# Kernel tuning notes

Hardware: AMD Instinct MI355X
Metric: run time of the kernel (lower is better)

## Reference

```python
import jax, jax.numpy as jnp
import numpy as np

NT = 128          # num_timesteps (reference query points)
E = 128           # embed_time
H = 128           # nhidden
NH = 1            # num_heads
F = 32            # feature_size
NS = 2            # num_states
EPS = 1e-5


def layer_norm(x, g, b):
    m = jnp.mean(x, axis=-1, keepdims=True)
    v = jnp.mean((x - m) ** 2, axis=-1, keepdims=True)
    return (x - m) * jax.lax.rsqrt(v + EPS) * g + b


def setup_inputs() -> dict:
    key = jax.random.key(0)
    ks = jax.random.split(key, 24)
    nrm = lambda k, s: (jax.random.normal(k, s) * 0.05).astype(jnp.float32)
    inp = {
        "input": jax.random.normal(ks[0], (8, F, 512), dtype=jnp.float32),
        "mask": jax.random.randint(ks[1], (8, F, 512), 0, 2).astype(jnp.float32),
        "timesteps": jnp.sort(jax.random.uniform(ks[2], (8, 512), dtype=jnp.float32), axis=-1),
        # time embedding
        "periodic_w": nrm(ks[3], (E - 1, 1)), "periodic_b": nrm(ks[4], (E - 1,)),
        "lin_w": nrm(ks[5], (1, 1)), "lin_b": nrm(ks[6], (1,)),
        # query / key projections + layer norms
        "q_w": nrm(ks[7], (E, E)), "q_b": nrm(ks[8], (E,)),
        "q_g": jnp.ones((E,), jnp.float32), "q_be": jnp.zeros((E,), jnp.float32),
        "k_w": nrm(ks[9], (E, E)), "k_b": nrm(ks[10], (E,)),
        "k_g": jnp.ones((E,), jnp.float32), "k_be": jnp.zeros((E,), jnp.float32),
        # attention_norm over h*2F channels, then output linear + LN to nhidden
        "attn_g": jnp.ones((NH * 2 * F,), jnp.float32), "attn_b": jnp.zeros((NH * 2 * F,), jnp.float32),
        "out_w": nrm(ks[11], (H, NH * 2 * F)), "out_b": nrm(ks[12], (H,)),
        "out_g": jnp.ones((H,), jnp.float32), "out_be": jnp.zeros((H,), jnp.float32),
        # GRU (torch gate order r, z, n)
        "gru_wih": nrm(ks[13], (3 * H, H)), "gru_whh": nrm(ks[14], (3 * H, H)),
        "gru_bih": nrm(ks[15], (3 * H,)), "gru_bhh": nrm(ks[16], (3 * H,)),
        # classifier MLP
        "c1_w": nrm(ks[17], (H, H)), "c1_b": nrm(ks[18], (H,)),
        "c2_w": nrm(ks[19], (H, H)), "c2_b": nrm(ks[20], (H,)),
        "c3_w": nrm(ks[21], (NS, H)), "c3_b": nrm(ks[22], (NS,)),
    }
    return inp


def time_embedding(tt, lin_w, lin_b, periodic_w, periodic_b):
    t = tt[..., None]                                   # (..., 1)
    out1 = t @ lin_w.T + lin_b                          # (..., 1)
    out2 = jnp.sin(t @ periodic_w.T + periodic_b)       # (..., E-1)
    return jnp.concatenate([out1, out2], axis=-1)       # (..., E)


def reference(input, mask, timesteps, periodic_w, periodic_b, lin_w, lin_b,
              q_w, q_b, q_g, q_be, k_w, k_b, k_g, k_be,
              attn_g, attn_b, out_w, out_b, out_g, out_be,
              gru_wih, gru_whh, gru_bih, gru_bhh,
              c1_w, c1_b, c2_w, c2_b, c3_w, c3_b):
    B = input.shape[0]
    x_in = jnp.transpose(input, (0, 2, 1))              # (B, T, F)
    m = 1.0 - jnp.transpose(mask, (0, 2, 1))            # (B, T, F)
    x_in = x_in * (m > 0).astype(x_in.dtype)
    x = jnp.concatenate([x_in, m], axis=-1)             # (B, T, 2F)
    mk = jnp.concatenate([m, m], axis=-1)               # (B, T, 2F)

    key_e = time_embedding(timesteps, lin_w, lin_b, periodic_w, periodic_b)        # (B, T, E)
    qtimes = jnp.linspace(0.0, 1.0, NT)
    query_e = time_embedding(qtimes[None], lin_w, lin_b, periodic_w, periodic_b)   # (1, NT, E)

    q = layer_norm(query_e @ q_w.T + q_b, q_g, q_be)    # (1, NT, E)
    k = layer_norm(key_e @ k_w.T + k_b, k_g, k_be)      # (B, T, E)

    etk = E // NH
    q = q.reshape(1, NT, NH, etk).transpose(0, 2, 1, 3)         # (1, h, NT, etk)
    k = k.reshape(B, -1, NH, etk).transpose(0, 2, 1, 3)         # (B, h, T, etk)

    scores = jnp.einsum("ahqd,bhkd->bhqk", q, k) / np.sqrt(etk)  # (B, h, NT, T)
    # per-channel masked softmax over keys: (B, h, NT, T, 2F)
    logits = jnp.where(mk[:, None, None, :, :] == 0, -1e9, scores[..., None])
    p_attn = jax.nn.softmax(logits, axis=-2)
    att = jnp.sum(p_attn * x[:, None, None, :, :], axis=-2)     # (B, h, NT, 2F)

    x2 = att.transpose(0, 2, 1, 3).reshape(B, NT, NH * 2 * F)
    x2 = layer_norm(x2, attn_g, attn_b)
    out = layer_norm(x2 @ out_w.T + out_b, out_g, out_be)       # (B, NT, H)

    # GRU over the NT reference timesteps, last hidden state
    seq = out.transpose(1, 0, 2)                                # (NT, B, H)
    h0 = jnp.zeros((B, H), out.dtype)

    def gru_step(h, x_t):
        gi = x_t @ gru_wih.T + gru_bih
        gh = h @ gru_whh.T + gru_bhh
        ir, iz, inn = jnp.split(gi, 3, axis=-1)
        hr, hz, hn = jnp.split(gh, 3, axis=-1)
        r = jax.nn.sigmoid(ir + hr)
        z = jax.nn.sigmoid(iz + hz)
        n = jnp.tanh(inn + r * hn)
        h_new = (1.0 - z) * n + z * h
        return h_new, None

    h_last, _ = jax.lax.scan(gru_step, h0, seq)

    h1 = jax.nn.relu(h_last @ c1_w.T + c1_b)
    h2 = jax.nn.relu(h1 @ c2_w.T + c2_b)
    return h2 @ c3_w.T + c3_b                                   # (B, num_states) logits
```

## Files before the change

kernel.cpp:

```cpp
#include <hip/hip_runtime.h>
#include <math.h>

#define LN_EPS 1e-5f

typedef _Float16 h2v __attribute__((ext_vector_type(2)));

__device__ __forceinline__ float dot4(float4 a, float4 b) {
    return a.x*b.x + a.y*b.y + a.z*b.z + a.w*b.w;
}
__device__ __forceinline__ void fma4(float4& a, float s, float4 v) {
    a.x += s*v.x; a.y += s*v.y; a.z += s*v.z; a.w += s*v.w;
}
__device__ __forceinline__ float fast_rcp(float x) {
    return __builtin_amdgcn_rcpf(x);
}
__device__ __forceinline__ float fast_sigmoid(float x) {
    return fast_rcp(1.f + __expf(-x));
}
__device__ __forceinline__ float fast_tanh(float x) {
    return 1.f - 2.f*fast_rcp(__expf(2.f*x) + 1.f);
}
__device__ __forceinline__ float fdot2u(unsigned int a, unsigned int b, float c) {
#if __has_builtin(__builtin_amdgcn_fdot2)
    return __builtin_amdgcn_fdot2(__builtin_bit_cast(h2v, a),
                                  __builtin_bit_cast(h2v, b), c, false);
#else
    const h2v av = __builtin_bit_cast(h2v, a);
    const h2v bv = __builtin_bit_cast(h2v, b);
    return c + (float)av[0]*(float)bv[0] + (float)av[1]*(float)bv[1];
#endif
}
__device__ __forceinline__ float wsum64(float v) {
    #pragma unroll
    for (int off = 32; off > 0; off >>= 1) v += __shfl_xor(v, off);
    return v;
}
__device__ __forceinline__ float qadd_xor1(float v) {
    const int x = __builtin_amdgcn_mov_dpp(__builtin_bit_cast(int, v),
                                           0xB1 , 0xF, 0xF, true);
    return v + __builtin_bit_cast(float, x);
}

__global__ void k_embed_proj(
    const float* __restrict__ input, const float* __restrict__ mask,
    const float* __restrict__ timesteps,
    const float* __restrict__ pw, const float* __restrict__ pb,
    const float* __restrict__ lw, const float* __restrict__ lb,
    const float* __restrict__ q_w, const float* __restrict__ q_b,
    const float* __restrict__ q_g, const float* __restrict__ q_be,
    const float* __restrict__ k_w, const float* __restrict__ k_b,
    const float* __restrict__ k_g, const float* __restrict__ k_be,
    float* __restrict__ qs, float* __restrict__ kT, float2* __restrict__ xm)
{
    const int blk = blockIdx.x;
    const int tid = threadIdx.x;

    __shared__ __align__(16) float e[4][128];
    __shared__ __align__(16) float4 red[128];
    __shared__ __align__(16) float proj[4][128];
    __shared__ __align__(16) float2 tile[32][65];

    if (blk < 64) {
        const int b  = blk >> 3;
        const int t0 = (blk & 7) * 64;
        const int cg = tid >> 6;
        const int tt = tid & 63;
        #pragma unroll
        for (int c16 = 0; c16 < 16; ++c16) {
            const int c = c16*2 + cg;
            const float m = mask [(size_t)(b*32 + c)*512 + t0 + tt];
            const float x = input[(size_t)(b*32 + c)*512 + t0 + tt];
            const float mm = 1.0f - m;
            tile[c][tt] = make_float2(x*mm, mm);
        }
        __syncthreads();
        const int c2 = tid & 31;
        const int tg = tid >> 5;
        #pragma unroll
        for (int k = 0; k < 16; ++k) {
            const int t = tg*16 + k;
            xm[((size_t)b*512 + t0 + t)*32 + c2] = tile[c2][t];
        }
        return;
    }

    const bool isq = blk < 96;
    float tv[4];
    int kidx0 = 0;
    if (isq) {
        const int q0 = (blk - 64) * 4;
        #pragma unroll
        for (int r = 0; r < 4; ++r) tv[r] = (float)(q0 + r) * (1.0f/127.0f);
    } else {
        kidx0 = (blk - 96) * 4;
        #pragma unroll
        for (int r = 0; r < 4; ++r) tv[r] = timesteps[kidx0 + r];
    }

    float pwj = 0.f, pbj = 0.f;
    if (tid > 0) { pwj = pw[tid-1]; pbj = pb[tid-1]; }
    const float lw0 = lw[0], lb0 = lb[0];
    #pragma unroll
    for (int r = 0; r < 4; ++r)
        e[r][tid] = (tid == 0) ? (tv[r]*lw0 + lb0) : sinf(tv[r]*pwj + pbj);
    __syncthreads();

    const float* W  = isq ? q_w  : k_w;
    const float* Bv = isq ? q_b  : k_b;
    const float* G  = isq ? q_g  : k_g;
    const float* Be = isq ? q_be : k_be;

    {
        const int jj = tid >> 2, dc = tid & 3;
        const float4* e0 = (const float4*)(&e[0][0]);
        const float4* e1 = (const float4*)(&e[1][0]);
        const float4* e2 = (const float4*)(&e[2][0]);
        const float4* e3 = (const float4*)(&e[3][0]);
        #pragma unroll
        for (int jb = 0; jb < 4; ++jb) {
            const int j = jb*32 + jj;
            const float4* wrow = (const float4*)(W + (size_t)j*128);
            float a0=0.f, a1=0.f, a2=0.f, a3=0.f;
            #pragma unroll
            for (int k = 0; k < 8; ++k) {
                const int idx = dc + 4*k;
                const float4 w4 = wrow[idx];
                a0 += dot4(w4, e0[idx]);
                a1 += dot4(w4, e1[idx]);
                a2 += dot4(w4, e2[idx]);
                a3 += dot4(w4, e3[idx]);
            }
            a0 += __shfl_xor(a0, 1, 4); a0 += __shfl_xor(a0, 2, 4);
            a1 += __shfl_xor(a1, 1, 4); a1 += __shfl_xor(a1, 2, 4);
            a2 += __shfl_xor(a2, 1, 4); a2 += __shfl_xor(a2, 2, 4);
            a3 += __shfl_xor(a3, 1, 4); a3 += __shfl_xor(a3, 2, 4);
            if (dc == 0) {
                const float bj = Bv[j];
                proj[0][j] = a0 + bj; proj[1][j] = a1 + bj;
                proj[2][j] = a2 + bj; proj[3][j] = a3 + bj;
            }
        }
    }
    __syncthreads();

    float acc[4];
    #pragma unroll
    for (int r = 0; r < 4; ++r) acc[r] = proj[r][tid];

    red[tid] = make_float4(acc[0], acc[1], acc[2], acc[3]);
    __syncthreads();
    for (int s = 64; s > 0; s >>= 1) {
        if (tid < s) {
            float4 m = red[tid]; const float4 o = red[tid+s];
            m.x += o.x; m.y += o.y; m.z += o.z; m.w += o.w;
            red[tid] = m;
        }
        __syncthreads();
    }
    float4 mean = red[0];
    mean.x *= (1.0f/128.0f); mean.y *= (1.0f/128.0f);
    mean.z *= (1.0f/128.0f); mean.w *= (1.0f/128.0f);
    __syncthreads();
    const float d0 = acc[0]-mean.x, d1 = acc[1]-mean.y,
                d2 = acc[2]-mean.z, d3 = acc[3]-mean.w;
    red[tid] = make_float4(d0*d0, d1*d1, d2*d2, d3*d3);
    __syncthreads();
    for (int s = 64; s > 0; s >>= 1) {
        if (tid < s) {
            float4 m = red[tid]; const float4 o = red[tid+s];
            m.x += o.x; m.y += o.y; m.z += o.z; m.w += o.w;
            red[tid] = m;
        }
        __syncthreads();
    }
    float4 var = red[0];
    var.x *= (1.0f/128.0f); var.y *= (1.0f/128.0f);
    var.z *= (1.0f/128.0f); var.w *= (1.0f/128.0f);

    const float gg = G[tid], bb = Be[tid];
    const float o0 = d0*rsqrtf(var.x+LN_EPS)*gg + bb;
    const float o1 = d1*rsqrtf(var.y+LN_EPS)*gg + bb;
    const float o2 = d2*rsqrtf(var.z+LN_EPS)*gg + bb;
    const float o3 = d3*rsqrtf(var.w+LN_EPS)*gg + bb;

    if (isq) {
        const float sc = 0.08838834764831845f;
        const int q0 = (blk - 64)*4;
        qs[(size_t)(q0+0)*128 + tid] = o0*sc;
        qs[(size_t)(q0+1)*128 + tid] = o1*sc;
        qs[(size_t)(q0+2)*128 + tid] = o2*sc;
        qs[(size_t)(q0+3)*128 + tid] = o3*sc;
    } else {
        const int b = kidx0 >> 9;
        const int t = kidx0 & 511;
        *(float4*)(kT + ((size_t)(b*128 + tid))*512 + t) =
            make_float4(o0, o1, o2, o3);
    }
}

__global__ void __launch_bounds__(256) k_attn(
    const float2* __restrict__ xm,
    const float* __restrict__ qs, const float* __restrict__ kT,
    const float* __restrict__ attn_g, const float* __restrict__ attn_b,
    const float* __restrict__ out_w, const float* __restrict__ out_b,
    const float* __restrict__ out_g, const float* __restrict__ out_be,
    float* __restrict__ outm)
{
    const int b     = blockIdx.x >> 5;
    const int qbase = (blockIdx.x & 31) * 4;
    const int tid   = threadIdx.x;

    __shared__ __align__(16) float et[4][512];
    __shared__ __align__(16) float qsh[4][128];
    __shared__ __align__(16) float wsh[128*66];
    __shared__ __align__(16) float sA[4][8][32];
    __shared__ __align__(16) float aA[4][8][32];
    __shared__ __align__(16) float x2s[4][64];
    __shared__ float redC[4];

    for (int idx = tid; idx < 512; idx += 256)
        qsh[idx >> 7][idx & 127] = qs[(size_t)(qbase + (idx >> 7))*128 + (idx & 127)];
    for (int idx = tid; idx < 8192; idx += 256)
        wsh[(idx >> 6)*66 + (idx & 63)] = out_w[idx];
    __syncthreads();

    {
        const int grp = tid >> 7;
        const int tl  = tid & 127;
        const int q0  = grp*2;
        const float4* kp  = (const float4*)kT + (size_t)b*128*128 + tl;
        const float4* qa4 = (const float4*)qsh[q0];
        const float4* qb4 = (const float4*)qsh[q0+1];
        float4 a0 = make_float4(0,0,0,0), a1 = make_float4(0,0,0,0);
        float4 c0 = kp[0], c1 = kp[128], c2 = kp[256], c3 = kp[384];
        for (int c = 0; c < 32; ++c) {
            float4 n0, n1, n2, n3;
            if (c < 31) {
                const float4* kn = kp + (size_t)(4*c+4)*128;
                n0 = kn[0]; n1 = kn[128]; n2 = kn[256]; n3 = kn[384];
            }
            const float4 qa = qa4[c], qb = qb4[c];
            fma4(a0, qa.x, c0); fma4(a1, qb.x, c0);
            fma4(a0, qa.y, c1); fma4(a1, qb.y, c1);
            fma4(a0, qa.z, c2); fma4(a1, qb.z, c2);
            fma4(a0, qa.w, c3); fma4(a1, qb.w, c3);
            c0 = n0; c1 = n1; c2 = n2; c3 = n3;
        }
        a0.x = __expf(a0.x); a0.y = __expf(a0.y); a0.z = __expf(a0.z); a0.w = __expf(a0.w);
        a1.x = __expf(a1.x); a1.y = __expf(a1.y); a1.z = __expf(a1.z); a1.w = __expf(a1.w);
        ((float4*)et[q0])[tl]   = a0;
        ((float4*)et[q0+1])[tl] = a1;
    }
    __syncthreads();

    {
        const int c   = tid & 31;
        const int seg = tid >> 5;
        const float2* xp = xm + ((size_t)b*512 + seg*64)*32 + c;
        float s0=0,s1=0,s2=0,s3=0, a0=0,a1=0,a2=0,a3=0;
        #pragma unroll 4
        for (int i = 0; i < 64; ++i) {
            const float2 v = xp[(size_t)i*32];
            const int t = seg*64 + i;
            const float w0 = et[0][t]*v.y, w1 = et[1][t]*v.y;
            const float w2 = et[2][t]*v.y, w3 = et[3][t]*v.y;
            s0 += w0; s1 += w1; s2 += w2; s3 += w3;
            a0 += w0*v.x; a1 += w1*v.x; a2 += w2*v.x; a3 += w3*v.x;
        }
        sA[0][seg][c]=s0; sA[1][seg][c]=s1; sA[2][seg][c]=s2; sA[3][seg][c]=s3;
        aA[0][seg][c]=a0; aA[1][seg][c]=a1; aA[2][seg][c]=a2; aA[3][seg][c]=a3;
    }
    __syncthreads();

    {
        const int ql = tid >> 6;
        const int c2 = tid & 63;
        const int cc = c2 & 31;
        float ss = 0.f;
        #pragma unroll
        for (int g = 0; g < 8; ++g) ss += sA[ql][g][cc];
        float attv;
        if (c2 < 32) {
            float aa = 0.f;
            #pragma unroll
            for (int g = 0; g < 8; ++g) aa += aA[ql][g][cc];
            attv = (ss > 0.f) ? aa/ss : 0.f;
        } else {
            attv = (ss > 0.f) ? 1.0f : 0.0f;
        }
        const float mean = wsum64(attv) * (1.0f/64.0f);
        const float dv = attv - mean;
        const float var = wsum64(dv*dv) * (1.0f/64.0f);
        x2s[ql][c2] = dv*rsqrtf(var+LN_EPS)*attn_g[c2] + attn_b[c2];
    }
    __syncthreads();

    {
        const int jhalf = tid >> 7;
        const int j     = tid & 127;
        const int wave  = tid >> 6;
        for (int lq2 = 0; lq2 < 2; ++lq2) {
            const int ql = jhalf*2 + lq2;
            float acc = out_b[j];
            const float4* wrow = (const float4*)(wsh + j*66);
            const float4* xr   = (const float4*)x2s[ql];
            #pragma unroll
            for (int k = 0; k < 16; ++k) acc += dot4(wrow[k], xr[k]);

            float v = wsum64(acc);
            if ((tid & 63) == 0) redC[wave] = v;
            __syncthreads();
            const float mean = (redC[jhalf*2] + redC[jhalf*2+1]) * (1.0f/128.0f);
            __syncthreads();
            const float d = acc - mean;
            v = wsum64(d*d);
            if ((tid & 63) == 0) redC[wave] = v;
            __syncthreads();
            const float var = (redC[jhalf*2] + redC[jhalf*2+1]) * (1.0f/128.0f);
            outm[((size_t)b*128 + qbase + ql)*128 + j] =
                d*rsqrtf(var+LN_EPS)*out_g[j] + out_be[j];
            __syncthreads();
        }
    }
}

__global__ void k_gi(const float* __restrict__ outm,
                     const float* __restrict__ wih, const float* __restrict__ bih,
                     float* __restrict__ gi)
{
    const int qi  = blockIdx.x;
    const int tid = threadIdx.x;
    __shared__ __align__(16) float rows[8][128];
    for (int idx = tid; idx < 1024; idx += 384) {
        const int b = idx >> 7, d = idx & 127;
        rows[b][d] = outm[(size_t)(b*128+qi)*128 + d];
    }
    __syncthreads();

    const int g0 = tid >> 2, dc = tid & 3;
    #pragma unroll
    for (int gb = 0; gb < 4; ++gb) {
        const int g = gb*96 + g0;
        const float4* wrow = (const float4*)(wih + (size_t)g*128);
        float acc[8] = {0,0,0,0,0,0,0,0};
        #pragma unroll
        for (int k = 0; k < 8; ++k) {
            const int idx = dc + 4*k;
            const float4 w4 = wrow[idx];
            #pragma unroll
            for (int b = 0; b < 8; ++b)
                acc[b] += dot4(w4, ((const float4*)rows[b])[idx]);
        }
        #pragma unroll
        for (int b = 0; b < 8; ++b) {
            acc[b] += __shfl_xor(acc[b], 1, 4);
            acc[b] += __shfl_xor(acc[b], 2, 4);
        }
        if (dc == 0) {
            const float bi = bih[g];
            #pragma unroll
            for (int b = 0; b < 8; ++b)
                gi[((size_t)qi*8 + b)*384 + g] = acc[b] + bi;
        }
    }
}

__global__ void __launch_bounds__(256) k_gru_cls(
    const float* __restrict__ gi,
    const float* __restrict__ whh, const float* __restrict__ bhh,
    const float* __restrict__ c1w, const float* __restrict__ c1b,
    const float* __restrict__ c2w, const float* __restrict__ c2b,
    const float* __restrict__ c3w, const float* __restrict__ c3b,
    float* __restrict__ out)
{
    const int b   = blockIdx.x;
    const int tid = threadIdx.x;
    const int u   = tid >> 1;
    const int s   = tid & 1;

    __shared__ __align__(16) _Float16 hbuf[2][128];
    __shared__ __align__(16) float hcls[128];
    __shared__ __align__(16) float scr[256];

    unsigned int wreg[3][32];
    #pragma unroll
    for (int g = 0; g < 3; ++g) {
        const float4* wrow = (const float4*)(whh + (size_t)(g*128 + u)*128 + 64*s);
        #pragma unroll
        for (int i = 0; i < 16; ++i) {
            const float4 v = wrow[i];
            h2v p0; p0[0] = (_Float16)v.x; p0[1] = (_Float16)v.y;
            h2v p1; p1[0] = (_Float16)v.z; p1[1] = (_Float16)v.w;
            wreg[g][2*i]   = __builtin_bit_cast(unsigned int, p0);
            wreg[g][2*i+1] = __builtin_bit_cast(unsigned int, p1);
        }
    }
    const float bh_r = bhh[u], bh_z = bhh[u+128], bh_n = bhh[u+256];

    const float* gpR = gi + (size_t)b*384 + u;
    const float* gpZ = gpR + 128;
    const float* gpN = gpR + 256;

    float gR[4], gZ[4], gN[4];
    #pragma unroll
    for (int j = 0; j < 4; ++j) {
        gR[j] = gpR[(size_t)j*3072];
        gZ[j] = gpZ[(size_t)j*3072];
        gN[j] = gpN[(size_t)j*3072];
    }

    if (tid < 128) { hbuf[0][tid] = (_Float16)0.f; hbuf[1][tid] = (_Float16)0.f; }
    float hprev = 0.f;
    __syncthreads();

#define GRU_BODY(RB, WB, J, PF)                                                \
    {                                                                          \
        const float giR = gR[J], giZ = gZ[J], giN = gN[J];                     \
        gR[J] = gpR[(size_t)(PF)*3072];                                        \
        gZ[J] = gpZ[(size_t)(PF)*3072];                                        \
        gN[J] = gpN[(size_t)(PF)*3072];                                        \
        const uint4* hp4 = (const uint4*)&hbuf[RB][0] + s*8;                   \
        uint4 hv[8];                                                           \
        _Pragma("unroll")                                                      \
        for (int i = 0; i < 8; ++i) hv[i] = hp4[i];                            \
        float ar[2] = {0.f,0.f}, az[2] = {0.f,0.f}, an[2] = {0.f,0.f};         \
        _Pragma("unroll")                                                      \
        for (int i = 0; i < 8; ++i) {                                          \
            const int p = i >> 2;                                              \
            ar[p] = fdot2u(wreg[0][4*i+0], hv[i].x, ar[p]);                    \
            ar[p] = fdot2u(wreg[0][4*i+1], hv[i].y, ar[p]);                    \
            ar[p] = fdot2u(wreg[0][4*i+2], hv[i].z, ar[p]);                    \
            ar[p] = fdot2u(wreg[0][4*i+3], hv[i].w, ar[p]);                    \
            az[p] = fdot2u(wreg[1][4*i+0], hv[i].x, az[p]);                    \
            az[p] = fdot2u(wreg[1][4*i+1], hv[i].y, az[p]);                    \
            az[p] = fdot2u(wreg[1][4*i+2], hv[i].z, az[p]);                    \
            az[p] = fdot2u(wreg[1][4*i+3], hv[i].w, az[p]);                    \
            an[p] = fdot2u(wreg[2][4*i+0], hv[i].x, an[p]);                    \
            an[p] = fdot2u(wreg[2][4*i+1], hv[i].y, an[p]);                    \
            an[p] = fdot2u(wreg[2][4*i+2], hv[i].z, an[p]);                    \
            an[p] = fdot2u(wreg[2][4*i+3], hv[i].w, an[p]);                    \
        }                                                                      \
        float arr = qadd_xor1(ar[0] + ar[1]);                                  \
        float azz = qadd_xor1(az[0] + az[1]);                                  \
        float ann = qadd_xor1(an[0] + an[1]);                                  \
        const float r = fast_sigmoid(giR + arr + bh_r);                        \
        const float z = fast_sigmoid(giZ + azz + bh_z);                        \
        const float n = fast_tanh(giN + r*(ann + bh_n));                       \
        hprev = (1.f - z)*n + z*hprev;                                         \
        if (s == 0) hbuf[WB][u] = (_Float16)hprev;                             \
    }

    #pragma unroll 1
    for (int qi = 0; qi < 128; qi += 4) {
        GRU_BODY(0, 1, 0, (qi+4 < 128 ? qi+4 : 127));
        __syncthreads();
        GRU_BODY(1, 0, 1, (qi+5 < 128 ? qi+5 : 127));
        __syncthreads();
        GRU_BODY(0, 1, 2, (qi+6 < 128 ? qi+6 : 127));
        __syncthreads();
        GRU_BODY(1, 0, 3, (qi+7 < 128 ? qi+7 : 127));
        __syncthreads();
    }
#undef GRU_BODY

    if (s == 0) hcls[u] = hprev;
    __syncthreads();
    if (tid < 128) {
        float acc = c1b[tid];
        const float4* wc = (const float4*)(c1w + (size_t)tid*128);
        const float4* v  = (const float4*)hcls;
        #pragma unroll
        for (int d4 = 0; d4 < 32; ++d4) acc += dot4(wc[d4], v[d4]);
        scr[tid] = fmaxf(acc, 0.f);
    }
    __syncthreads();
    if (tid < 128) {
        float acc = c2b[tid];
        const float4* wc = (const float4*)(c2w + (size_t)tid*128);
        const float4* v  = (const float4*)scr;
        #pragma unroll
        for (int d4 = 0; d4 < 32; ++d4) acc += dot4(wc[d4], v[d4]);
        scr[128 + tid] = fmaxf(acc, 0.f);
    }
    __syncthreads();
    if (tid < 2) {
        float acc = c3b[tid];
        const float4* wc = (const float4*)(c3w + (size_t)tid*128);
        const float4* v  = (const float4*)(scr + 128);
        #pragma unroll
        for (int d4 = 0; d4 < 32; ++d4) acc += dot4(wc[d4], v[d4]);
        out[(size_t)b*2 + tid] = acc;
    }
}

extern "C" void kernel_launch(void* const* d_in, const int* in_sizes, int n_in,
                              void* d_out, int out_size, void* d_ws, size_t ws_size,
                              hipStream_t stream)
{
    const float* input     = (const float*)d_in[0];
    const float* mask      = (const float*)d_in[1];
    const float* timesteps = (const float*)d_in[2];
    const float* pw        = (const float*)d_in[3];
    const float* pb        = (const float*)d_in[4];
    const float* lw        = (const float*)d_in[5];
    const float* lb        = (const float*)d_in[6];
    const float* q_w       = (const float*)d_in[7];
    const float* q_b       = (const float*)d_in[8];
    const float* q_g       = (const float*)d_in[9];
    const float* q_be      = (const float*)d_in[10];
    const float* k_w       = (const float*)d_in[11];
    const float* k_b       = (const float*)d_in[12];
    const float* k_g       = (const float*)d_in[13];
    const float* k_be      = (const float*)d_in[14];
    const float* attn_g    = (const float*)d_in[15];
    const float* attn_b    = (const float*)d_in[16];
    const float* out_w     = (const float*)d_in[17];
    const float* out_b     = (const float*)d_in[18];
    const float* out_g     = (const float*)d_in[19];
    const float* out_be    = (const float*)d_in[20];
    const float* gru_wih   = (const float*)d_in[21];
    const float* gru_whh   = (const float*)d_in[22];
    const float* gru_bih   = (const float*)d_in[23];
    const float* gru_bhh   = (const float*)d_in[24];
    const float* c1_w      = (const float*)d_in[25];
    const float* c1_b      = (const float*)d_in[26];
    const float* c2_w      = (const float*)d_in[27];
    const float* c2_b      = (const float*)d_in[28];
    const float* c3_w      = (const float*)d_in[29];
    const float* c3_b      = (const float*)d_in[30];

    float* ws   = (float*)d_ws;
    float*  qs   = ws;
    float*  kT   = qs   + 16384;
    float*  outm = kT   + 524288;
    float*  gi   = outm + 131072;
    float2* xm   = (float2*)(gi + 393216);

    k_embed_proj<<<1120, 128, 0, stream>>>(input, mask, timesteps,
                                           pw, pb, lw, lb,
                                           q_w, q_b, q_g, q_be,
                                           k_w, k_b, k_g, k_be, qs, kT, xm);
    k_attn<<<256, 256, 0, stream>>>(xm, qs, kT,
                                    attn_g, attn_b, out_w, out_b,
                                    out_g, out_be, outm);
    k_gi<<<128, 384, 0, stream>>>(outm, gru_wih, gru_bih, gi);
    k_gru_cls<<<8, 256, 0, stream>>>(gi, gru_whh, gru_bhh,
                                     c1_w, c1_b, c2_w, c2_b, c3_w, c3_b,
                                     (float*)d_out);
}
```

Measured before the change: 220.3 us.

## Fuse GRU input projection into attention kernel and batch 16 rows per embed block

The GRU input-gate projection (k_gi) is folded into the tail of k_attn, so the layer-normed output rows stay in shared memory and are never written to or re-read from global memory. One kernel launch is removed. The embedding/projection kernel now handles 16 rows per block instead of 4, which cuts the block count. Its tree reductions become wave-level sums, and it uses the fast __sinf intrinsic. The out_w staging load is moved after the score computation. The trade-offs are higher register use and lower precision in the sine.

```diff
diff --git a/kernel.cpp b/kernel.cpp
--- a/kernel.cpp
+++ b/kernel.cpp
@@ -55,10 +55,11 @@
     const int blk = blockIdx.x;
     const int tid = threadIdx.x;
 
-    __shared__ __align__(16) float e[4][128];
-    __shared__ __align__(16) float4 red[128];
-    __shared__ __align__(16) float proj[4][128];
+    __shared__ __align__(16) float e[16][128];
+    __shared__ __align__(16) float proj[16][128];
     __shared__ __align__(16) float2 tile[32][65];
+    __shared__ __align__(16) float red2[2][16];
+    __shared__ __align__(16) float red2b[2][16];
 
     if (blk < 64) {
         const int b  = blk >> 3;
@@ -84,25 +85,25 @@
         return;
     }
 
-    const bool isq = blk < 96;
-    float tv[4];
-    int kidx0 = 0;
+    const bool isq = blk < 72;
+    float tv[16];
+    int kidx0 = 0, q0 = 0;
     if (isq) {
-        const int q0 = (blk - 64) * 4;
-        #pragma unroll
-        for (int r = 0; r < 4; ++r) tv[r] = (float)(q0 + r) * (1.0f/127.0f);
+        q0 = (blk - 64) * 16;
+        #pragma unroll
+        for (int r = 0; r < 16; ++r) tv[r] = (float)(q0 + r) * (1.0f/127.0f);
     } else {
-        kidx0 = (blk - 96) * 4;
-        #pragma unroll
-        for (int r = 0; r < 4; ++r) tv[r] = timesteps[kidx0 + r];
+        kidx0 = (blk - 72) * 16;
+        #pragma unroll
+        for (int r = 0; r < 16; ++r) tv[r] = timesteps[kidx0 + r];
     }
 
     float pwj = 0.f, pbj = 0.f;
     if (tid > 0) { pwj = pw[tid-1]; pbj = pb[tid-1]; }
     const float lw0 = lw[0], lb0 = lb[0];
     #pragma unroll
-    for (int r = 0; r < 4; ++r)
-        e[r][tid] = (tid == 0) ? (tv[r]*lw0 + lb0) : sinf(tv[r]*pwj + pbj);
+    for (int r = 0; r < 16; ++r)
+        e[r][tid] = (tid == 0) ? (tv[r]*lw0 + lb0) : __sinf(tv[r]*pwj + pbj);
     __syncthreads();
 
     const float* W  = isq ? q_w  : k_w;
@@ -112,89 +113,77 @@
 
     {
         const int jj = tid >> 2, dc = tid & 3;
-        const float4* e0 = (const float4*)(&e[0][0]);
-        const float4* e1 = (const float4*)(&e[1][0]);
-        const float4* e2 = (const float4*)(&e[2][0]);
-        const float4* e3 = (const float4*)(&e[3][0]);
         #pragma unroll
         for (int jb = 0; jb < 4; ++jb) {
             const int j = jb*32 + jj;
             const float4* wrow = (const float4*)(W + (size_t)j*128);
-            float a0=0.f, a1=0.f, a2=0.f, a3=0.f;
+            float a[16];
+            #pragma unroll
+            for (int r = 0; r < 16; ++r) a[r] = 0.f;
             #pragma unroll
             for (int k = 0; k < 8; ++k) {
                 const int idx = dc + 4*k;
                 const float4 w4 = wrow[idx];
-                a0 += dot4(w4, e0[idx]);
-                a1 += dot4(w4, e1[idx]);
-                a2 += dot4(w4, e2[idx]);
-                a3 += dot4(w4, e3[idx]);
-            }
-            a0 += __shfl_xor(a0, 1, 4); a0 += __shfl_xor(a0, 2, 4);
-            a1 += __shfl_xor(a1, 1, 4); a1 += __shfl_xor(a1, 2, 4);
-            a2 += __shfl_xor(a2, 1, 4); a2 += __shfl_xor(a2, 2, 4);
-            a3 += __shfl_xor(a3, 1, 4); a3 += __shfl_xor(a3, 2, 4);
+                #pragma unroll
+                for (int r = 0; r < 16; ++r)
+                    a[r] += dot4(w4, ((const float4*)e[r])[idx]);
+            }
+            #pragma unroll
+            for (int r = 0; r < 16; ++r) {
+                a[r] += __shfl_xor(a[r], 1, 4);
+                a[r] += __shfl_xor(a[r], 2, 4);
+            }
             if (dc == 0) {
                 const float bj = Bv[j];
-                proj[0][j] = a0 + bj; proj[1][j] = a1 + bj;
-                proj[2][j] = a2 + bj; proj[3][j] = a3 + bj;
-            }
-        }
-    }
-    __syncthreads();
-
-    float acc[4];
-    #pragma unroll
-    for (int r = 0; r < 4; ++r) acc[r] = proj[r][tid];
-
-    red[tid] = make_float4(acc[0], acc[1], acc[2], acc[3]);
-    __syncthreads();
-    for (int s = 64; s > 0; s >>= 1) {
-        if (tid < s) {
-            float4 m = red[tid]; const float4 o = red[tid+s];
-            m.x += o.x; m.y += o.y; m.z += o.z; m.w += o.w;
-            red[tid] = m;
-        }
-        __syncthreads();
-    }
-    float4 mean = red[0];
-    mean.x *= (1.0f/128.0f); mean.y *= (1.0f/128.0f);
-    mean.z *= (1.0f/128.0f); mean.w *= (1.0f/128.0f);
-    __syncthreads();
-    const float d0 = acc[0]-mean.x, d1 = acc[1]-mean.y,
-                d2 = acc[2]-mean.z, d3 = acc[3]-mean.w;
-    red[tid] = make_float4(d0*d0, d1*d1, d2*d2, d3*d3);
-    __syncthreads();
-    for (int s = 64; s > 0; s >>= 1) {
-        if (tid < s) {
-            float4 m = red[tid]; const float4 o = red[tid+s];
-            m.x += o.x; m.y += o.y; m.z += o.z; m.w += o.w;
-            red[tid] = m;
-        }
-        __syncthreads();
-    }
-    float4 var = red[0];
-    var.x *= (1.0f/128.0f); var.y *= (1.0f/128.0f);
-    var.z *= (1.0f/128.0f); var.w *= (1.0f/128.0f);
+                #pragma unroll
+                for (int r = 0; r < 16; ++r) proj[r][j] = a[r] + bj;
+            }
+        }
+    }
+    __syncthreads();
+
+    float acc[16];
+    #pragma unroll
+    for (int r = 0; r < 16; ++r) acc[r] = proj[r][tid];
+
+    #pragma unroll
+    for (int r = 0; r < 16; ++r) {
+        const float m = wsum64(acc[r]);
+        if ((tid & 63) == 0) red2[tid >> 6][r] = m;
+    }
+    __syncthreads();
+    float d[16];
+    #pragma unroll
+    for (int r = 0; r < 16; ++r)
+        d[r] = acc[r] - (red2[0][r] + red2[1][r]) * (1.0f/128.0f);
+    #pragma unroll
+    for (int r = 0; r < 16; ++r) {
+        const float v = wsum64(d[r]*d[r]);
+        if ((tid & 63) == 0) red2b[tid >> 6][r] = v;
+    }
+    __syncthreads();
 
     const float gg = G[tid], bb = Be[tid];
-    const float o0 = d0*rsqrtf(var.x+LN_EPS)*gg + bb;
-    const float o1 = d1*rsqrtf(var.y+LN_EPS)*gg + bb;
-    const float o2 = d2*rsqrtf(var.z+LN_EPS)*gg + bb;
-    const float o3 = d3*rsqrtf(var.w+LN_EPS)*gg + bb;
+    float o[16];
+    #pragma unroll
+    for (int r = 0; r < 16; ++r) {
+        const float var = (red2b[0][r] + red2b[1][r]) * (1.0f/128.0f);
+        o[r] = d[r]*rsqrtf(var+LN_EPS)*gg + bb;
+    }
 
     if (isq) {
         const float sc = 0.08838834764831845f;
-        const int q0 = (blk - 64)*4;
-        qs[(size_t)(q0+0)*128 + tid] = o0*sc;
-        qs[(size_t)(q0+1)*128 + tid] = o1*sc;
-        qs[(size_t)(q0+2)*128 + tid] = o2*sc;
-        qs[(size_t)(q0+3)*128 + tid] = o3*sc;
+        #pragma unroll
+        for (int r = 0; r < 16; ++r)
+            qs[(size_t)(q0+r)*128 + tid] = o[r]*sc;
     } else {
         const int b = kidx0 >> 9;
         const int t = kidx0 & 511;
-        *(float4*)(kT + ((size_t)(b*128 + tid))*512 + t) =
-            make_float4(o0, o1, o2, o3);
+        float* dst = kT + ((size_t)(b*128 + tid))*512 + t;
+        *(float4*)(dst)      = make_float4(o[0],  o[1],  o[2],  o[3]);
+        *(float4*)(dst + 4)  = make_float4(o[4],  o[5],  o[6],  o[7]);
+        *(float4*)(dst + 8)  = make_float4(o[8],  o[9],  o[10], o[11]);
+        *(float4*)(dst + 12) = make_float4(o[12], o[13], o[14], o[15]);
     }
 }
 
@@ -204,7 +193,8 @@
     const float* __restrict__ attn_g, const float* __restrict__ attn_b,
     const float* __restrict__ out_w, const float* __restrict__ out_b,
     const float* __restrict__ out_g, const float* __restrict__ out_be,
-    float* __restrict__ outm)
+    const float* __restrict__ wih, const float* __restrict__ bih,
+    float* __restrict__ gi)
 {
     const int b     = blockIdx.x >> 5;
     const int qbase = (blockIdx.x & 31) * 4;
@@ -216,12 +206,11 @@
     __shared__ __align__(16) float sA[4][8][32];
     __shared__ __align__(16) float aA[4][8][32];
     __shared__ __align__(16) float x2s[4][64];
+    __shared__ __align__(16) float om[4][128];
     __shared__ float redC[4];
 
     for (int idx = tid; idx < 512; idx += 256)
         qsh[idx >> 7][idx & 127] = qs[(size_t)(qbase + (idx >> 7))*128 + (idx & 127)];
-    for (int idx = tid; idx < 8192; idx += 256)
-        wsh[(idx >> 6)*66 + (idx & 63)] = out_w[idx];
     __syncthreads();
 
     {
@@ -251,6 +240,8 @@
         ((float4*)et[q0])[tl]   = a0;
         ((float4*)et[q0+1])[tl] = a1;
     }
+    for (int idx = tid; idx < 8192; idx += 256)
+        wsh[(idx >> 6)*66 + (idx & 63)] = out_w[idx];
     __syncthreads();
 
     {
@@ -317,50 +308,38 @@
             if ((tid & 63) == 0) redC[wave] = v;
             __syncthreads();
             const float var = (redC[jhalf*2] + redC[jhalf*2+1]) * (1.0f/128.0f);
-            outm[((size_t)b*128 + qbase + ql)*128 + j] =
-                d*rsqrtf(var+LN_EPS)*out_g[j] + out_be[j];
+            om[ql][j] = d*rsqrtf(var+LN_EPS)*out_g[j] + out_be[j];
             __syncthreads();
         }
     }
-}
-
-__global__ void k_gi(const float* __restrict__ outm,
-                     const float* __restrict__ wih, const float* __restrict__ bih,
-                     float* __restrict__ gi)
-{
-    const int qi  = blockIdx.x;
-    const int tid = threadIdx.x;
-    __shared__ __align__(16) float rows[8][128];
-    for (int idx = tid; idx < 1024; idx += 384) {
-        const int b = idx >> 7, d = idx & 127;
-        rows[b][d] = outm[(size_t)(b*128+qi)*128 + d];
-    }
-    __syncthreads();
-
-    const int g0 = tid >> 2, dc = tid & 3;
-    #pragma unroll
-    for (int gb = 0; gb < 4; ++gb) {
-        const int g = gb*96 + g0;
-        const float4* wrow = (const float4*)(wih + (size_t)g*128);
-        float acc[8] = {0,0,0,0,0,0,0,0};
-        #pragma unroll
-        for (int k = 0; k < 8; ++k) {
-            const int idx = dc + 4*k;
-            const float4 w4 = wrow[idx];
-            #pragma unroll
-            for (int b = 0; b < 8; ++b)
-                acc[b] += dot4(w4, ((const float4*)rows[b])[idx]);
-        }
-        #pragma unroll
-        for (int b = 0; b < 8; ++b) {
-            acc[b] += __shfl_xor(acc[b], 1, 4);
-            acc[b] += __shfl_xor(acc[b], 2, 4);
-        }
-        if (dc == 0) {
-            const float bi = bih[g];
-            #pragma unroll
-            for (int b = 0; b < 8; ++b)
-                gi[((size_t)qi*8 + b)*384 + g] = acc[b] + bi;
+
+    {
+        const int grp = tid >> 2;
+        const int dc  = tid & 3;
+        #pragma unroll
+        for (int gb = 0; gb < 6; ++gb) {
+            const int g = gb*64 + grp;
+            const float4* wrow = (const float4*)(wih + (size_t)g*128);
+            float acc[4] = {0,0,0,0};
+            #pragma unroll
+            for (int k = 0; k < 8; ++k) {
+                const int idx = dc + 4*k;
+                const float4 w4 = wrow[idx];
+                #pragma unroll
+                for (int ql = 0; ql < 4; ++ql)
+                    acc[ql] += dot4(w4, ((const float4*)om[ql])[idx]);
+            }
+            #pragma unroll
+            for (int ql = 0; ql < 4; ++ql) {
+                acc[ql] += __shfl_xor(acc[ql], 1, 4);
+                acc[ql] += __shfl_xor(acc[ql], 2, 4);
+            }
+            if (dc == 0) {
+                const float bi = bih[g];
+                #pragma unroll
+                for (int ql = 0; ql < 4; ++ql)
+                    gi[((size_t)(qbase+ql)*8 + b)*384 + g] = acc[ql] + bi;
+            }
         }
     }
 }
@@ -440,9 +419,9 @@
             an[p] = fdot2u(wreg[2][4*i+2], hv[i].z, an[p]);                    \
             an[p] = fdot2u(wreg[2][4*i+3], hv[i].w, an[p]);                    \
         }                                                                      \
-        float arr = qadd_xor1(ar[0] + ar[1]);                                  \
-        float azz = qadd_xor1(az[0] + az[1]);                                  \
-        float ann = qadd_xor1(an[0] + an[1]);                                  \
+        const float arr = qadd_xor1(ar[0] + ar[1]);                            \
+        const float azz = qadd_xor1(az[0] + az[1]);                            \
+        const float ann = qadd_xor1(an[0] + an[1]);                            \
         const float r = fast_sigmoid(giR + arr + bh_r);                        \
         const float z = fast_sigmoid(giZ + azz + bh_z);                        \
         const float n = fast_tanh(giN + r*(ann + bh_n));                       \
@@ -536,14 +515,13 @@
     float*  gi   = outm + 131072;
     float2* xm   = (float2*)(gi + 393216);
 
-    k_embed_proj<<<1120, 128, 0, stream>>>(input, mask, timesteps,
-                                           pw, pb, lw, lb,
-                                           q_w, q_b, q_g, q_be,
-                                           k_w, k_b, k_g, k_be, qs, kT, xm);
+    k_embed_proj<<<328, 128, 0, stream>>>(input, mask, timesteps,
+                                          pw, pb, lw, lb,
+                                          q_w, q_b, q_g, q_be,
+                                          k_w, k_b, k_g, k_be, qs, kT, xm);
     k_attn<<<256, 256, 0, stream>>>(xm, qs, kT,
                                     attn_g, attn_b, out_w, out_b,
-                                    out_g, out_be, outm);
-    k_gi<<<128, 384, 0, stream>>>(outm, gru_wih, gru_bih, gi);
+                                    out_g, out_be, gru_wih, gru_bih, gi);
     k_gru_cls<<<8, 256, 0, stream>>>(gi, gru_whh, gru_bhh,
                                      c1_w, c1_b, c2_w, c2_b, c3_w, c3_b,
                                      (float*)d_out);
```

After: 230.6 us. +4.7%, slower.
